# Kernel tuning notes

Measured on AMD Instinct MI355X. Metric: run time of the kernel, lower is better.

Reference implementation:

```python
import jax, jax.numpy as jnp
import numpy as np

B, IN_DIM, C, H, W = 4, 64, 128, 64, 64
HW = H * W
EPS = 1e-5


def _conv(x, w, b, pad):
    y = jax.lax.conv_general_dilated(
        x, w, (1, 1), [(pad, pad), (pad, pad)],
        dimension_numbers=('NCHW', 'OIHW', 'NCHW'))
    return y + b[None, :, None, None]


def _ln_chw(x, g, b):
    # torch LayerNorm([C,H,W]): normalize over (C,H,W) per sample, affine per-element
    m = jnp.mean(x, axis=(1, 2, 3), keepdims=True)
    v = jnp.mean((x - m) ** 2, axis=(1, 2, 3), keepdims=True)
    return (x - m) * jax.lax.rsqrt(v + EPS) * g[None] + b[None]


def _lrelu(x):
    return jnp.where(x >= 0, x, 0.01 * x)


def setup_inputs():
    ks = jax.random.split(jax.random.key(0), 16)

    def n(i, shape, s):
        return jax.random.normal(ks[i], shape, jnp.float32) * s

    inp = {
        'f_e': n(0, (B, IN_DIM, H, W), 1.0),
        'f_i': n(1, (B, IN_DIM, H, W), 1.0),
        'w1': n(2, (C, IN_DIM, 3, 3), 0.04), 'b1': jnp.zeros((C,), jnp.float32),
        'g1': jnp.ones((C, H, W), jnp.float32), 'be1': jnp.zeros((C, H, W), jnp.float32),
        'w2': n(3, (C, IN_DIM, 3, 3), 0.04), 'b2': jnp.zeros((C,), jnp.float32),
        'g2': jnp.ones((C, H, W), jnp.float32), 'be2': jnp.zeros((C, H, W), jnp.float32),
        'W3': n(4, (HW, HW), 0.015), 'b3': jnp.zeros((HW,), jnp.float32),
        'W4': n(5, (C, C), 0.08), 'b4': jnp.zeros((C,), jnp.float32),
        'W5': n(6, (C, C), 0.08), 'b5': jnp.zeros((C,), jnp.float32),
        'w6a': n(7, (C, C, 1, 1), 0.08), 'b6a': jnp.zeros((C,), jnp.float32),
        'g6a': jnp.ones((C, H, W), jnp.float32), 'be6a': jnp.zeros((C, H, W), jnp.float32),
        'w6b': n(8, (C, C, 3, 3), 0.03), 'b6b': jnp.zeros((C,), jnp.float32),
        'g6b': jnp.ones((C, H, W), jnp.float32), 'be6b': jnp.zeros((C, H, W), jnp.float32),
        'wf': n(9, (IN_DIM, C, 1, 1), 0.08), 'bf': jnp.zeros((IN_DIM,), jnp.float32),
    }
    return inp


def reference(f_e, f_i, w1, b1, g1, be1, w2, b2, g2, be2, W3, b3, W4, b4,
              W5, b5, w6a, b6a, g6a, be6a, w6b, b6b, g6b, be6b, wf, bf):
    b_, _, h, w = f_e.shape
    c = w1.shape[0]
    hw = h * w

    # f_1: conv3x3 -> LN([C,H,W]) -> LeakyReLU -> b (hw) c
    x1 = _lrelu(_ln_chw(_conv(f_e, w1, b1, 1), g1, be1))
    f_e_1 = x1.transpose(0, 2, 3, 1).reshape(b_, hw, c)

    # f_2: conv3x3 -> LN -> LeakyReLU (stays b c h w)
    f_i_2 = _lrelu(_ln_chw(_conv(f_i, w2, b2, 1), g2, be2))

    # f_3: b c (hw) -> Linear(HW,HW) -> LeakyReLU
    f_i_3 = _lrelu(jnp.einsum('bcn,mn->bcm', f_i_2.reshape(b_, c, hw), W3) + b3)

    # f_4: b (hw) c -> Linear(C,C) -> LeakyReLU
    tok = f_i_2.transpose(0, 2, 3, 1).reshape(b_, hw, c)
    f_e_4 = _lrelu(jnp.einsum('bnc,dc->bnd', tok, W4) + b4)

    # unscaled single-head attention over hw tokens
    scores = jnp.einsum('bnc,bcm->bnm', f_e_4, f_i_3)   # (b, hw, hw)
    attn = jax.nn.softmax(scores, axis=-1)
    f_e_5_in = jnp.einsum('bnm,bmc->bnc', attn, f_e_1)

    # f_5: Linear(C,C) -> LeakyReLU -> b c h w
    f_e_5 = _lrelu(jnp.einsum('bnc,dc->bnd', f_e_5_in, W5) + b5)
    f_e_5 = f_e_5.reshape(b_, h, w, c).transpose(0, 3, 1, 2)

    # f_6: conv1x1 -> LN -> LReLU -> conv3x3 -> LN -> LReLU
    y = _lrelu(_ln_chw(_conv(f_i_2, w6a, b6a, 0), g6a, be6a))
    f_i_6 = _lrelu(_ln_chw(_conv(y, w6b, b6b, 1), g6b, be6b))

    f_e_7 = f_e_5 * f_i_6
    f_e_8 = _conv(f_e_7, wf, bf, 0)
    return (f_e_8, f_i_2)
```

## Files before the change

### kernel.cpp

```cpp
#include <hip/hip_runtime.h>

typedef unsigned short ushort_t;
typedef unsigned int uint_t;
typedef unsigned long long u64_t;

#define Bn 4
#define IND 64
#define Cn 128
#define Nn 4096
#define CN 524288
#define BUF 2097152

typedef __attribute__((ext_vector_type(8))) __bf16 bf16x8;
typedef __attribute__((ext_vector_type(4))) float f32x4;

__device__ __forceinline__ float b2f(ushort_t s) {
    return __uint_as_float(((uint_t)s) << 16);
}
__device__ __forceinline__ ushort_t f2b(float f) {
    uint_t u = __float_as_uint(f);
    uint_t r = u + 0x7fffu + ((u >> 16) & 1u);
    return (ushort_t)(r >> 16);
}
__device__ __forceinline__ void unpack8(uint4 u, float* f) {
    f[0] = __uint_as_float(u.x << 16); f[1] = __uint_as_float(u.x & 0xffff0000u);
    f[2] = __uint_as_float(u.y << 16); f[3] = __uint_as_float(u.y & 0xffff0000u);
    f[4] = __uint_as_float(u.z << 16); f[5] = __uint_as_float(u.z & 0xffff0000u);
    f[6] = __uint_as_float(u.w << 16); f[7] = __uint_as_float(u.w & 0xffff0000u);
}
__device__ __forceinline__ float lrelu(float x) { return x >= 0.f ? x : 0.01f * x; }

__device__ __forceinline__ float getv(const float* p, size_t i) { return p[i]; }
__device__ __forceinline__ float getv(const ushort_t* p, size_t i) { return b2f(p[i]); }
__device__ __forceinline__ float4 get4(const float* p, size_t i) { return *(const float4*)(p + i); }
__device__ __forceinline__ float4 get4(const ushort_t* p, size_t i) {
    ushort4 u = *(const ushort4*)(p + i);
    float4 f = {b2f(u.x), b2f(u.y), b2f(u.z), b2f(u.w)};
    return f;
}
__device__ __forceinline__ void stv(float* p, float v) { *p = v; }
__device__ __forceinline__ void stv(ushort_t* p, float v) { *p = f2b(v); }

__device__ __forceinline__ uint4 pack8(float4 a, float4 b) {
    uint4 r;
    r.x = (uint_t)f2b(a.x) | ((uint_t)f2b(a.y) << 16);
    r.y = (uint_t)f2b(a.z) | ((uint_t)f2b(a.w) << 16);
    r.z = (uint_t)f2b(b.x) | ((uint_t)f2b(b.y) << 16);
    r.w = (uint_t)f2b(b.z) | ((uint_t)f2b(b.w) << 16);
    return r;
}

__global__ void detect_kernel(const void* g1, int* flag) {
    if (threadIdx.x == 0 && blockIdx.x == 0)
        *flag = (((const ushort_t*)g1)[0] == 0x3F80) ? 0 : 1;
}

template <int CI>
__global__ __launch_bounds__(256) void wtrans(const void* w, ushort_t* Wt, const int* flagp) {
    int F = *flagp;
    int idx = blockIdx.x * 256 + threadIdx.x;
    if (idx >= 128 * 9 * CI) return;
    int co = idx / (9 * CI);
    int rem = idx - co * 9 * CI;
    int tap = rem / CI;
    int ci = rem - tap * CI;
    size_t srci = (size_t)co * CI * 9 + (size_t)ci * 9 + tap;
    float v = F ? ((const float*)w)[srci] : b2f(((const ushort_t*)w)[srci]);
    Wt[idx] = f2b(v);
}

template <typename TEXT>
__device__ __forceinline__ void tin_body(const TEXT* src, ushort_t* dst, float (*tile)[33]) {
    int b = blockIdx.z, c0 = blockIdx.y * 32, n0 = blockIdx.x * 32;
    int nx = threadIdx.x & 31, cy = threadIdx.x >> 5;
    #pragma unroll
    for (int s = 0; s < 4; s++) {
        int cl = cy + s * 8;
        tile[cl][nx] = getv(src, ((size_t)(b * 64 + c0 + cl)) * 4096 + n0 + nx);
    }
    __syncthreads();
    #pragma unroll
    for (int s = 0; s < 4; s++) {
        int nl = cy + s * 8;
        dst[((size_t)b * 4096 + n0 + nl) * 64 + c0 + nx] = f2b(tile[nx][nl]);
    }
}

__global__ __launch_bounds__(256) void transpose_in(const void* src, ushort_t* dst, const int* flagp) {
    __shared__ float tile[32][33];
    int F = *flagp;
    if (F) tin_body((const float*)src, dst, tile);
    else   tin_body((const ushort_t*)src, dst, tile);
}

template <int CI>
__global__ __launch_bounds__(512) void conv_mfma(const ushort_t* __restrict__ Xt,
                                                 const ushort_t* __restrict__ Wt,
                                                 const void* bias, float* __restrict__ out,
                                                 const int* flagp) {
    constexpr int RS = CI + 8;
    constexpr int SROWS = 195;
    constexpr int SBYTES = SROWS * RS * 2;
    constexpr int OBYTES = 128 * 68 * 4;
    constexpr int SMEM = SBYTES > OBYTES ? SBYTES : OBYTES;
    __shared__ __align__(16) char smem[SMEM];
    ushort_t* S = (ushort_t*)smem;
    float* Ob = (float*)smem;

    int t = threadIdx.x;
    int blk = blockIdx.x;
    int b = blk >> 6, y = blk & 63;
    int n0 = y << 6;

    constexpr int RQ = CI / 8;
    constexpr int CNT = SROWS * RQ;
    for (int i = t; i < CNT; i += 512) {
        int s = i / RQ;
        int c8 = (i - s * RQ) * 8;
        int tok = n0 + s - 65;
        uint4 v = {0u, 0u, 0u, 0u};
        if (s < 194 && (unsigned)tok < 4096u)
            v = *(const uint4*)(Xt + ((size_t)b * 4096 + tok) * CI + c8);
        *(uint4*)(S + (size_t)s * RS + c8) = v;
    }
    __syncthreads();

    int lane = t & 63, w = t >> 6;
    int li = lane & 15, q = lane >> 4;
    int px0 = 16 * (w & 3);
    int coh = 64 * (w >> 2);
    int x = px0 + li;

    f32x4 acc[4];
    #pragma unroll
    for (int T = 0; T < 4; T++) acc[T] = {0.f, 0.f, 0.f, 0.f};

    #pragma unroll
    for (int tap = 0; tap < 9; tap++) {
        int dy = tap / 3 - 1, dx = tap % 3 - 1;
        bool vx = (unsigned)(x + dx) < 64u;
        int srow = x + dy * 64 + dx + 65;
        int sr2 = vx ? srow : 194;
        #pragma unroll
        for (int ks = 0; ks < CI / 32; ks++) {
            bf16x8 a = *(const bf16x8*)(S + (size_t)sr2 * RS + ks * 32 + q * 8);
            #pragma unroll
            for (int T = 0; T < 4; T++) {
                int co = coh + 16 * T + li;
                bf16x8 bb = *(const bf16x8*)(Wt + ((size_t)co * 9 + tap) * CI + ks * 32 + q * 8);
                acc[T] = __builtin_amdgcn_mfma_f32_16x16x32_bf16(a, bb, acc[T], 0, 0, 0);
            }
        }
    }
    __syncthreads();

    int F = *flagp;
    #pragma unroll
    for (int T = 0; T < 4; T++) {
        int co = coh + 16 * T + li;
        float bv = F ? ((const float*)bias)[co] : b2f(((const ushort_t*)bias)[co]);
        #pragma unroll
        for (int rr = 0; rr < 4; rr++)
            Ob[(size_t)co * 68 + px0 + 4 * q + rr] = acc[T][rr] + bv;
    }
    __syncthreads();
    for (int i = t; i < 2048; i += 512) {
        int co = i >> 4, p4 = (i & 15) * 4;
        *(uint4*)(out + ((size_t)(b * 128 + co)) * 4096 + n0 + p4) =
            *(const uint4*)(Ob + (size_t)co * 68 + p4);
    }
}

__global__ __launch_bounds__(256) void ln_reduce1(const float* __restrict__ src,
                                                  float* __restrict__ part) {
    int t = threadIdx.x;
    size_t base = (size_t)blockIdx.x * 1024 + t * 4;
    float4 v = *(const float4*)(src + base);
    float s = v.x + v.y + v.z + v.w;
    float q = v.x * v.x + v.y * v.y + v.z * v.z + v.w * v.w;
    for (int off = 32; off > 0; off >>= 1) {
        s += __shfl_down(s, off, 64);
        q += __shfl_down(q, off, 64);
    }
    __shared__ float red[8];
    if ((t & 63) == 0) { red[(t >> 6) * 2] = s; red[(t >> 6) * 2 + 1] = q; }
    __syncthreads();
    if (t == 0) {
        s = red[0] + red[2] + red[4] + red[6];
        q = red[1] + red[3] + red[5] + red[7];
        part[blockIdx.x * 2] = s;
        part[blockIdx.x * 2 + 1] = q;
    }
}

__global__ __launch_bounds__(256) void ln_reduce2(const float* __restrict__ part,
                                                  float* __restrict__ der) {
    int b = blockIdx.x, t = threadIdx.x;
    float s = part[(b * 512 + t) * 2] + part[(b * 512 + 256 + t) * 2];
    float q = part[(b * 512 + t) * 2 + 1] + part[(b * 512 + 256 + t) * 2 + 1];
    for (int off = 32; off > 0; off >>= 1) {
        s += __shfl_down(s, off, 64);
        q += __shfl_down(q, off, 64);
    }
    __shared__ float red[8];
    if ((t & 63) == 0) { red[(t >> 6) * 2] = s; red[(t >> 6) * 2 + 1] = q; }
    __syncthreads();
    if (t == 0) {
        s = red[0] + red[2] + red[4] + red[6];
        q = red[1] + red[3] + red[5] + red[7];
        float mean = s * (1.f / (float)CN);
        float var = q * (1.f / (float)CN) - mean * mean;
        der[b * 2] = mean;
        der[b * 2 + 1] = rsqrtf(var + 1e-5f);
    }
}

template <typename TEXT, typename TOD, int HT, int HD>
__device__ __forceinline__ void ln_body(const float* src, const TEXT* g, const TEXT* be,
                                        const float* der, ushort_t* outT, TOD* outD,
                                        float (*tile)[33]) {
    int b = blockIdx.z, c0 = blockIdx.y * 32, n0 = blockIdx.x * 32;
    float mean = der[b * 2], rstd = der[b * 2 + 1];
    int nx = threadIdx.x & 31, cy = threadIdx.x >> 5;
    #pragma unroll
    for (int s = 0; s < 4; s++) {
        int cl = cy + s * 8;
        int c = c0 + cl;
        size_t gi = (size_t)c * Nn + n0 + nx;
        float v = (src[(size_t)b * CN + gi] - mean) * rstd * getv(g, gi) + getv(be, gi);
        v = lrelu(v);
        if (HD) stv(outD + (size_t)b * CN + gi, v);
        tile[cl][nx] = v;
    }
    if (HT) {
        __syncthreads();
        #pragma unroll
        for (int s = 0; s < 4; s++) {
            int nl = cy + s * 8;
            int n = n0 + nl;
            int c = c0 + nx;
            outT[((size_t)b * Nn + n) * Cn + c] = f2b(tile[nx][nl]);
        }
    }
}

template <int HT, int HD, int DEXT>
__global__ __launch_bounds__(256) void ln_apply(const float* src, const void* g, const void* be,
                                                const float* der, ushort_t* outT, void* outD,
                                                long doff, const int* flagp) {
    __shared__ float tile[32][33];
    int F = *flagp;
    if (F) {
        if (DEXT && HD)
            ln_body<float, float, HT, HD>(src, (const float*)g, (const float*)be, der, outT,
                                          ((float*)outD) + doff, tile);
        else
            ln_body<float, ushort_t, HT, HD>(src, (const float*)g, (const float*)be, der, outT,
                                             ((ushort_t*)outD) + doff, tile);
    } else {
        ln_body<ushort_t, ushort_t, HT, HD>(src, (const ushort_t*)g, (const ushort_t*)be, der, outT,
                                            ((ushort_t*)outD) + doff, tile);
    }
}

template <int ACT, int TRANS, typename TA, typename TW, typename TO>
__device__ __forceinline__ void gemm_body(const TA* A, const TW* W, const TW* bias, TO* out,
                                          int M, int K, int Rper,
                                          float (*As)[68], float (*Bs)[68]) {
    int m0 = blockIdx.x << 6, r0 = blockIdx.y << 6;
    int t = threadIdx.x, tx = t & 15, ty = t >> 4;
    int sr = t >> 2, sk = (t & 3) << 2;
    float acc[4][4] = {{0.f}};
    for (int kt = 0; kt < K; kt += 16) {
        float4 av = get4(A, (size_t)(r0 + sr) * K + kt + sk);
        float4 wv = get4(W, (size_t)(m0 + sr) * K + kt + sk);
        As[sk + 0][sr] = av.x; As[sk + 1][sr] = av.y;
        As[sk + 2][sr] = av.z; As[sk + 3][sr] = av.w;
        Bs[sk + 0][sr] = wv.x; Bs[sk + 1][sr] = wv.y;
        Bs[sk + 2][sr] = wv.z; Bs[sk + 3][sr] = wv.w;
        __syncthreads();
        #pragma unroll
        for (int kk = 0; kk < 16; kk++) {
            float4 a4 = *(const float4*)&As[kk][ty << 2];
            float4 b4 = *(const float4*)&Bs[kk][tx << 2];
            float aa[4] = {a4.x, a4.y, a4.z, a4.w};
            float bb[4] = {b4.x, b4.y, b4.z, b4.w};
            #pragma unroll
            for (int ii = 0; ii < 4; ii++)
                #pragma unroll
                for (int jj = 0; jj < 4; jj++)
                    acc[ii][jj] += aa[ii] * bb[jj];
        }
        __syncthreads();
    }
    float bv[4];
    #pragma unroll
    for (int jj = 0; jj < 4; jj++) bv[jj] = getv(bias, m0 + (tx << 2) + jj);
    #pragma unroll
    for (int ii = 0; ii < 4; ii++) {
        int r = r0 + (ty << 2) + ii;
        float v[4];
        #pragma unroll
        for (int jj = 0; jj < 4; jj++) {
            float x = acc[ii][jj] + bv[jj];
            if (ACT) x = lrelu(x);
            v[jj] = x;
        }
        if (TRANS) {
            int rb = r / Rper, ri = r % Rper;
            #pragma unroll
            for (int jj = 0; jj < 4; jj++) {
                int m = m0 + (tx << 2) + jj;
                stv(out + ((size_t)rb * M + m) * Rper + ri, v[jj]);
            }
        } else {
            #pragma unroll
            for (int jj = 0; jj < 4; jj++)
                stv(out + (size_t)r * M + m0 + (tx << 2) + jj, v[jj]);
        }
    }
}

template <int ACT, int TRANS, int AK, typename TO>
__global__ __launch_bounds__(256) void gemm_nt(const void* A, long aoff, const void* W,
                                               const void* bias, TO* out, int M, int K, int Rper,
                                               const int* flagp) {
    __shared__ float As[16][68];
    __shared__ float Bs[16][68];
    int F = *flagp;
    if (AK == 0) {
        if (F) gemm_body<ACT, TRANS>((const ushort_t*)A + aoff, (const float*)W, (const float*)bias, out, M, K, Rper, As, Bs);
        else   gemm_body<ACT, TRANS>((const ushort_t*)A + aoff, (const ushort_t*)W, (const ushort_t*)bias, out, M, K, Rper, As, Bs);
    } else if (AK == 1) {
        if (F) gemm_body<ACT, TRANS>((const float*)A + aoff, (const float*)W, (const float*)bias, out, M, K, Rper, As, Bs);
        else   gemm_body<ACT, TRANS>((const float*)A + aoff, (const ushort_t*)W, (const ushort_t*)bias, out, M, K, Rper, As, Bs);
    } else {
        if (F) gemm_body<ACT, TRANS>((const float*)A + aoff, (const float*)W, (const float*)bias, out, M, K, Rper, As, Bs);
        else   gemm_body<ACT, TRANS>((const ushort_t*)A + aoff, (const ushort_t*)W, (const ushort_t*)bias, out, M, K, Rper, As, Bs);
    }
}

template <typename TA, typename TW>
__device__ __forceinline__ void gemm_big_body(const TA* A, const TW* W3, const TW* b3,
                                              ushort_t* out, char* smem) {
    ushort_t* As = (ushort_t*)smem;
    ushort_t* Bs = (ushort_t*)(smem + 9216);
    int t = threadIdx.x;
    int m0 = blockIdx.x << 7;
    int r0 = blockIdx.y << 6;
    int lane = t & 63, w = t >> 6;
    int li = lane & 15, q = lane >> 4;
    int rs = 16 * (w & 3);
    int mh = 64 * (w >> 2);
    f32x4 acc[4];
    #pragma unroll
    for (int T = 0; T < 4; T++) acc[T] = {0.f, 0.f, 0.f, 0.f};

    int ar = t >> 3, ak8 = (t & 7) * 8;
    int br = t >> 2, bk16 = (t & 3) * 16;

    {
        size_t abase = (size_t)(r0 + ar) * 4096 + ak8;
        *(uint4*)(As + (size_t)ar * 72 + ak8) = pack8(get4(A, abase), get4(A, abase + 4));
        size_t bbase = (size_t)(m0 + br) * 4096 + bk16;
        *(uint4*)(Bs + (size_t)br * 72 + bk16) = pack8(get4(W3, bbase), get4(W3, bbase + 4));
        *(uint4*)(Bs + (size_t)br * 72 + bk16 + 8) = pack8(get4(W3, bbase + 8), get4(W3, bbase + 12));
    }
    __syncthreads();

    for (int kt = 0; kt < 4096; kt += 64) {
        float4 pa0, pa1, pb0, pb1, pb2, pb3;
        bool pf = kt < 4032;
        if (pf) {
            size_t abase = (size_t)(r0 + ar) * 4096 + kt + 64 + ak8;
            pa0 = get4(A, abase); pa1 = get4(A, abase + 4);
            size_t bbase = (size_t)(m0 + br) * 4096 + kt + 64 + bk16;
            pb0 = get4(W3, bbase); pb1 = get4(W3, bbase + 4);
            pb2 = get4(W3, bbase + 8); pb3 = get4(W3, bbase + 12);
        }
        #pragma unroll
        for (int ks = 0; ks < 2; ks++) {
            bf16x8 a = *(const bf16x8*)(As + (size_t)(rs + li) * 72 + ks * 32 + q * 8);
            #pragma unroll
            for (int T = 0; T < 4; T++) {
                bf16x8 bb = *(const bf16x8*)(Bs + (size_t)(mh + 16 * T + li) * 72 + ks * 32 + q * 8);
                acc[T] = __builtin_amdgcn_mfma_f32_16x16x32_bf16(a, bb, acc[T], 0, 0, 0);
            }
        }
        __syncthreads();
        if (pf) {
            *(uint4*)(As + (size_t)ar * 72 + ak8) = pack8(pa0, pa1);
            *(uint4*)(Bs + (size_t)br * 72 + bk16) = pack8(pb0, pb1);
            *(uint4*)(Bs + (size_t)br * 72 + bk16 + 8) = pack8(pb2, pb3);
        }
        __syncthreads();
    }

    ushort_t* Ob = (ushort_t*)smem;
    #pragma unroll
    for (int T = 0; T < 4; T++) {
        int m_l = mh + 16 * T + li;
        float bv = getv(b3, m0 + m_l);
        #pragma unroll
        for (int rr = 0; rr < 4; rr++) {
            float v = lrelu(acc[T][rr] + bv);
            Ob[(size_t)m_l * 72 + rs + 4 * q + rr] = f2b(v);
        }
    }
    __syncthreads();
    int b = r0 >> 7;
    int c0 = ((r0 >> 6) & 1) * 64;
    for (int i = t; i < 1024; i += 512) {
        int m_l = i >> 3, c8 = (i & 7) * 8;
        *(uint4*)(out + ((size_t)b * 4096 + m0 + m_l) * 128 + c0 + c8) =
            *(const uint4*)(Ob + (size_t)m_l * 72 + c8);
    }
}

__global__ __launch_bounds__(512) void gemm_big(const void* A, long aoff, const void* W3,
                                                const void* b3, ushort_t* out, const int* flagp) {
    __shared__ __align__(16) char smem[27648];
    int F = *flagp;
    if (F) gemm_big_body((const float*)A + aoff, (const float*)W3, (const float*)b3, out, smem);
    else   gemm_big_body((const ushort_t*)A + aoff, (const ushort_t*)W3, (const ushort_t*)b3, out, smem);
}

__global__ __launch_bounds__(256) void attn_mfma(const ushort_t* __restrict__ Q,
                                                 const ushort_t* __restrict__ Kg,
                                                 const ushort_t* __restrict__ Vg,
                                                 float* __restrict__ Og) {
    __shared__ __align__(16) ushort_t Qs[64 * 136];
    __shared__ __align__(16) ushort_t Ks[64 * 136];
    __shared__ __align__(16) ushort_t Ps[64 * 72];
    __shared__ __align__(16) ushort_t Vt[128 * 68];

    int t = threadIdx.x;
    int blk = blockIdx.x;
    int b = (blk >> 1) & 3;
    int qt = ((blk >> 3) << 1) | (blk & 1);
    int n0 = qt << 6;
    int lane = t & 63, w = t >> 6;
    int li = lane & 15, q = lane >> 4;

    int kj = t >> 2, kc0 = (t & 3) * 32;
    int vd = t >> 1, vk0 = (t & 1) * 32;

    {
        const ushort_t* qp = Q + ((size_t)(b * Nn + n0 + kj)) * 128 + kc0;
        ushort_t* dst = Qs + kj * 136 + kc0;
        #pragma unroll
        for (int cc = 0; cc < 4; cc++)
            *(uint4*)(dst + cc * 8) = *(const uint4*)(qp + cc * 8);
    }
    {
        const ushort_t* kp = Kg + ((size_t)(b * Nn + kj)) * 128 + kc0;
        ushort_t* dst = Ks + kj * 136 + kc0;
        #pragma unroll
        for (int cc = 0; cc < 4; cc++)
            *(uint4*)(dst + cc * 8) = *(const uint4*)(kp + cc * 8);
    }
    {
        const ushort_t* vp = Vg + (size_t)b * CN + (size_t)vd * Nn + vk0;
        ushort_t* dst = Vt + vd * 68 + vk0;
        #pragma unroll
        for (int cc = 0; cc < 4; cc++) {
            uint4 v = *(const uint4*)(vp + cc * 8);
            uint2 lo = {v.x, v.y}, hi = {v.z, v.w};
            *(uint2*)(dst + cc * 8) = lo;
            *(uint2*)(dst + cc * 8 + 4) = hi;
        }
    }

    f32x4 acc[8];
    #pragma unroll
    for (int T = 0; T < 8; T++) acc[T] = {0.f, 0.f, 0.f, 0.f};
    float m_i[4], l_i[4];
    #pragma unroll
    for (int r = 0; r < 4; r++) { m_i[r] = -1e30f; l_i[r] = 0.f; }

    __syncthreads();

    for (int kt = 0; kt < 64; kt++) {
        uint4 pk[4], pv[4];
        bool pf = kt < 63;
        if (pf) {
            int m1 = (kt + 1) << 6;
            const ushort_t* kp = Kg + ((size_t)(b * Nn + m1 + kj)) * 128 + kc0;
            #pragma unroll
            for (int cc = 0; cc < 4; cc++) pk[cc] = *(const uint4*)(kp + cc * 8);
            const ushort_t* vp = Vg + (size_t)b * CN + (size_t)vd * Nn + m1 + vk0;
            #pragma unroll
            for (int cc = 0; cc < 4; cc++) pv[cc] = *(const uint4*)(vp + cc * 8);
        }

        f32x4 s[4];
        #pragma unroll
        for (int T = 0; T < 4; T++) s[T] = {0.f, 0.f, 0.f, 0.f};
        #pragma unroll
        for (int ks = 0; ks < 4; ks++) {
            bf16x8 a = *(const bf16x8*)(Qs + (16 * w + li) * 136 + ks * 32 + q * 8);
            #pragma unroll
            for (int T = 0; T < 4; T++) {
                bf16x8 bb = *(const bf16x8*)(Ks + (16 * T + li) * 136 + ks * 32 + q * 8);
                s[T] = __builtin_amdgcn_mfma_f32_16x16x32_bf16(a, bb, s[T], 0, 0, 0);
            }
        }

        float alpha[4];
        float p[4][4];
        #pragma unroll
        for (int r = 0; r < 4; r++) {
            float rm = fmaxf(fmaxf(s[0][r], s[1][r]), fmaxf(s[2][r], s[3][r]));
            rm = fmaxf(rm, __shfl_xor(rm, 1, 64));
            rm = fmaxf(rm, __shfl_xor(rm, 2, 64));
            rm = fmaxf(rm, __shfl_xor(rm, 4, 64));
            rm = fmaxf(rm, __shfl_xor(rm, 8, 64));
            float mnew = fmaxf(m_i[r], rm);
            alpha[r] = __expf(m_i[r] - mnew);
            m_i[r] = mnew;
            float rsum = 0.f;
            #pragma unroll
            for (int T = 0; T < 4; T++) {
                float pvv = __expf(s[T][r] - mnew);
                p[T][r] = pvv;
                rsum += pvv;
            }
            rsum += __shfl_xor(rsum, 1, 64);
            rsum += __shfl_xor(rsum, 2, 64);
            rsum += __shfl_xor(rsum, 4, 64);
            rsum += __shfl_xor(rsum, 8, 64);
            l_i[r] = l_i[r] * alpha[r] + rsum;
        }
        #pragma unroll
        for (int T = 0; T < 4; T++)
            #pragma unroll
            for (int r = 0; r < 4; r++)
                Ps[(16 * w + 4 * q + r) * 72 + 16 * T + li] = f2b(p[T][r]);

        #pragma unroll
        for (int T = 0; T < 8; T++)
            #pragma unroll
            for (int r = 0; r < 4; r++)
                acc[T][r] *= alpha[r];
        #pragma unroll
        for (int ks = 0; ks < 2; ks++) {
            bf16x8 a = *(const bf16x8*)(Ps + (16 * w + li) * 72 + ks * 32 + q * 8);
            #pragma unroll
            for (int T = 0; T < 8; T++) {
                const ushort_t* vb = Vt + (16 * T + li) * 68 + ks * 32 + q * 8;
                union { u64_t u[2]; bf16x8 v; } bv;
                bv.u[0] = *(const u64_t*)(vb);
                bv.u[1] = *(const u64_t*)(vb + 4);
                acc[T] = __builtin_amdgcn_mfma_f32_16x16x32_bf16(a, bv.v, acc[T], 0, 0, 0);
            }
        }
        __syncthreads();
        if (pf) {
            ushort_t* dk = Ks + kj * 136 + kc0;
            #pragma unroll
            for (int cc = 0; cc < 4; cc++) *(uint4*)(dk + cc * 8) = pk[cc];
            ushort_t* dv = Vt + vd * 68 + vk0;
            #pragma unroll
            for (int cc = 0; cc < 4; cc++) {
                uint2 lo = {pv[cc].x, pv[cc].y}, hi = {pv[cc].z, pv[cc].w};
                *(uint2*)(dv + cc * 8) = lo;
                *(uint2*)(dv + cc * 8 + 4) = hi;
            }
            __syncthreads();
        }
    }

    float inv[4];
    #pragma unroll
    for (int r = 0; r < 4; r++) inv[r] = 1.f / l_i[r];
    #pragma unroll
    for (int T = 0; T < 8; T++)
        #pragma unroll
        for (int r = 0; r < 4; r++) {
            int n = n0 + 16 * w + 4 * q + r;
            int d = 16 * T + li;
            Og[((size_t)(b * Nn + n)) * 128 + d] = acc[T][r] * inv[r];
        }
}

template <typename TEXT, typename TOUT>
__device__ __forceinline__ void final_body(const ushort_t* fe5, const ushort_t* fi6t,
                                           const TEXT* wf, const TEXT* bf, TOUT* out0,
                                           float* prod, ushort_t* wfs, float* bfs) {
    int t = threadIdx.x;
    int b = blockIdx.x >> 6;
    int px0 = (blockIdx.x & 63) * 64;
    for (int idx = t * 4; idx < 8192; idx += 1024) {
        float4 v = get4(wf, idx);
        ushort4 u = {f2b(v.x), f2b(v.y), f2b(v.z), f2b(v.w)};
        *(ushort4*)&wfs[idx] = u;
    }
    if (t < 64) bfs[t] = getv(bf, t);
    {
        int pix = t >> 2, kc = (t & 3) * 32;
        const ushort_t* ap = fe5 + ((size_t)(b * Nn + px0 + pix)) * 128 + kc;
        const ushort_t* bp = fi6t + ((size_t)(b * Nn + px0 + pix)) * 128 + kc;
        #pragma unroll
        for (int c = 0; c < 4; c++) {
            uint4 ua = *(const uint4*)(ap + c * 8);
            uint4 ub = *(const uint4*)(bp + c * 8);
            float fa[8], fb[8];
            unpack8(ua, fa);
            unpack8(ub, fb);
            float* pp = &prod[pix * 132 + kc + c * 8];
            #pragma unroll
            for (int j = 0; j < 8; j++) pp[j] = fa[j] * fb[j];
        }
    }
    __syncthreads();
    int pix = t >> 2, og = t & 3;
    for (int k = 0; k < 16; k++) {
        int o = og * 16 + k;
        float a = bfs[o];
        for (int kc = 0; kc < 128; kc += 8) {
            uint4 wu = *(const uint4*)&wfs[o * 128 + kc];
            float w8[8];
            unpack8(wu, w8);
            const float* pp = &prod[pix * 132 + kc];
            float4 p0 = *(const float4*)pp;
            float4 p1 = *(const float4*)(pp + 4);
            a += w8[0] * p0.x + w8[1] * p0.y + w8[2] * p0.z + w8[3] * p0.w
               + w8[4] * p1.x + w8[5] * p1.y + w8[6] * p1.z + w8[7] * p1.w;
        }
        stv(out0 + ((size_t)(b * 64 + o)) * Nn + px0 + pix, a);
    }
}

__global__ __launch_bounds__(256) void final_out(const ushort_t* fe5, const ushort_t* fi6t,
                                                 const void* wf, const void* bf, void* out0,
                                                 const int* flagp) {
    __shared__ __align__(16) float prod[64 * 132];
    __shared__ __align__(16) ushort_t wfs[64 * 128];
    __shared__ float bfs[64];
    int F = *flagp;
    if (F) final_body((const ushort_t*)fe5, fi6t, (const float*)wf, (const float*)bf, (float*)out0, prod, wfs, bfs);
    else   final_body((const ushort_t*)fe5, fi6t, (const ushort_t*)wf, (const ushort_t*)bf, (ushort_t*)out0, prod, wfs, bfs);
}

extern "C" void kernel_launch(void* const* d_in, const int* in_sizes, int n_in,
                              void* d_out, int out_size, void* d_ws, size_t ws_size,
                              hipStream_t stream) {
    const void* f_e = d_in[0];
    const void* f_i = d_in[1];
    const void* w1 = d_in[2];
    const void* b1 = d_in[3];
    const void* g1 = d_in[4];
    const void* be1 = d_in[5];
    const void* w2 = d_in[6];
    const void* b2 = d_in[7];
    const void* g2 = d_in[8];
    const void* be2 = d_in[9];
    const void* W3 = d_in[10];
    const void* b3 = d_in[11];
    const void* W4 = d_in[12];
    const void* b4 = d_in[13];
    const void* W5 = d_in[14];
    const void* b5 = d_in[15];
    const void* w6a = d_in[16];
    const void* b6a = d_in[17];
    const void* g6a = d_in[18];
    const void* be6a = d_in[19];
    const void* w6b = d_in[20];
    const void* b6b = d_in[21];
    const void* g6b = d_in[22];
    const void* be6b = d_in[23];
    const void* wf = d_in[24];
    const void* bf = d_in[25];

    char* wsb = (char*)d_ws;
    int* FLAG = (int*)wsb;
    float* PART = (float*)(wsb + 1024);
    float* DER  = (float*)(wsb + 17408);
    ushort_t* Wt1  = (ushort_t*)(wsb + 32768);
    ushort_t* Wt2  = (ushort_t*)(wsb + 180224);
    ushort_t* Wt6b = (ushort_t*)(wsb + 327680);
    float* TMP  = (float*)(wsb + 622592);
    ushort_t* FE1  = (ushort_t*)(wsb + 9011200);
    ushort_t* TOK  = FE1 + BUF;
    ushort_t* FI3T = TOK + BUF;
    ushort_t* FE4  = FI3T + BUF;
    ushort_t* Y6   = FE4 + BUF;
    ushort_t* FI6T = Y6 + BUF;

    ushort_t* FEt = FI3T;
    ushort_t* FIt = FE4;

    const long OUT1OFF = (long)Bn * IND * Nn;

    dim3 lnGrid(128, 4, 4);
    dim3 tinGrid(128, 2, 4);

    detect_kernel<<<1, 64, 0, stream>>>(g1, FLAG);

    wtrans<64><<<288, 256, 0, stream>>>(w1, Wt1, FLAG);
    wtrans<64><<<288, 256, 0, stream>>>(w2, Wt2, FLAG);
    wtrans<128><<<576, 256, 0, stream>>>(w6b, Wt6b, FLAG);

    transpose_in<<<tinGrid, 256, 0, stream>>>(f_e, FEt, FLAG);
    conv_mfma<64><<<256, 512, 0, stream>>>(FEt, Wt1, b1, TMP, FLAG);
    ln_reduce1<<<2048, 256, 0, stream>>>(TMP, PART);
    ln_reduce2<<<4, 256, 0, stream>>>(PART, DER);
    ln_apply<0, 1, 0><<<lnGrid, 256, 0, stream>>>(TMP, g1, be1, DER, nullptr, FE1, 0, FLAG);

    transpose_in<<<tinGrid, 256, 0, stream>>>(f_i, FIt, FLAG);
    conv_mfma<64><<<256, 512, 0, stream>>>(FIt, Wt2, b2, TMP, FLAG);
    ln_reduce1<<<2048, 256, 0, stream>>>(TMP, PART);
    ln_reduce2<<<4, 256, 0, stream>>>(PART, DER);
    ln_apply<1, 1, 1><<<lnGrid, 256, 0, stream>>>(TMP, g2, be2, DER, TOK, d_out, OUT1OFF, FLAG);

    gemm_big<<<dim3(32, 8), 512, 0, stream>>>(d_out, OUT1OFF, W3, b3, FI3T, FLAG);

    gemm_nt<1, 0, 0, ushort_t><<<dim3(2, 256), 256, 0, stream>>>(TOK, 0, W4, b4, FE4, 128, 128, 1, FLAG);

    gemm_nt<0, 1, 0, float><<<dim3(2, 256), 256, 0, stream>>>(TOK, 0, w6a, b6a, TMP, 128, 128, 4096, FLAG);
    ln_reduce1<<<2048, 256, 0, stream>>>(TMP, PART);
    ln_reduce2<<<4, 256, 0, stream>>>(PART, DER);
    ln_apply<1, 0, 0><<<lnGrid, 256, 0, stream>>>(TMP, g6a, be6a, DER, Y6, nullptr, 0, FLAG);

    conv_mfma<128><<<256, 512, 0, stream>>>(Y6, Wt6b, b6b, TMP, FLAG);
    ln_reduce1<<<2048, 256, 0, stream>>>(TMP, PART);
    ln_reduce2<<<4, 256, 0, stream>>>(PART, DER);
    ln_apply<1, 0, 0><<<lnGrid, 256, 0, stream>>>(TMP, g6b, be6b, DER, FI6T, nullptr, 0, FLAG);

    attn_mfma<<<256, 256, 0, stream>>>(FE4, FI3T, FE1, TMP);

    gemm_nt<1, 0, 1, ushort_t><<<dim3(2, 256), 256, 0, stream>>>(TMP, 0, W5, b5, Y6, 128, 128, 1, FLAG);

    final_out<<<256, 256, 0, stream>>>(Y6, FI6T, wf, bf, d_out, FLAG);
}
```

Before: 607.3 us.

## Split attention KV range in two and merge partial results

Splits the attention key/value loop into two halves handled by separate blocks, doubling the grid from 256 to 512 blocks. Each half writes unnormalized bf16 partial outputs plus per-row max and sum, and a new merge kernel combines them with log-sum-exp rescaling into the fp32 output. This targets low occupancy on a GPU with many compute units, at the cost of an extra kernel launch, extra memory traffic, and bf16 rounding of the unnormalized partial accumulators. The P tile's shared-memory stride also changes from 72 to 80.

New measurement: 592.7 us. 2.4% less time.

```diff
diff --git a/kernel.cpp b/kernel.cpp
--- a/kernel.cpp
+++ b/kernel.cpp
@@ -428,16 +428,20 @@
 __global__ __launch_bounds__(256) void attn_mfma(const ushort_t* __restrict__ Q,
                                                  const ushort_t* __restrict__ Kg,
                                                  const ushort_t* __restrict__ Vg,
-                                                 float* __restrict__ Og) {
+                                                 ushort_t* __restrict__ Op0,
+                                                 ushort_t* __restrict__ Op1,
+                                                 float* __restrict__ ML) {
     __shared__ __align__(16) ushort_t Qs[64 * 136];
     __shared__ __align__(16) ushort_t Ks[64 * 136];
-    __shared__ __align__(16) ushort_t Ps[64 * 72];
+    __shared__ __align__(16) ushort_t Ps[64 * 80];
     __shared__ __align__(16) ushort_t Vt[128 * 68];
 
     int t = threadIdx.x;
     int blk = blockIdx.x;
-    int b = (blk >> 1) & 3;
-    int qt = ((blk >> 3) << 1) | (blk & 1);
+    int h = blk >> 8;
+    int rblk = blk & 255;
+    int b = (rblk >> 1) & 3;
+    int qt = ((rblk >> 3) << 1) | (rblk & 1);
     int n0 = qt << 6;
     int lane = t & 63, w = t >> 6;
     int li = lane & 15, q = lane >> 4;
@@ -445,6 +449,9 @@
     int kj = t >> 2, kc0 = (t & 3) * 32;
     int vd = t >> 1, vk0 = (t & 1) * 32;
 
+    int kt0 = h << 5;
+    int m00 = kt0 << 6;
+
     {
         const ushort_t* qp = Q + ((size_t)(b * Nn + n0 + kj)) * 128 + kc0;
         ushort_t* dst = Qs + kj * 136 + kc0;
@@ -453,14 +460,14 @@
             *(uint4*)(dst + cc * 8) = *(const uint4*)(qp + cc * 8);
     }
     {
-        const ushort_t* kp = Kg + ((size_t)(b * Nn + kj)) * 128 + kc0;
+        const ushort_t* kp = Kg + ((size_t)(b * Nn + m00 + kj)) * 128 + kc0;
         ushort_t* dst = Ks + kj * 136 + kc0;
         #pragma unroll
         for (int cc = 0; cc < 4; cc++)
             *(uint4*)(dst + cc * 8) = *(const uint4*)(kp + cc * 8);
     }
     {
-        const ushort_t* vp = Vg + (size_t)b * CN + (size_t)vd * Nn + vk0;
+        const ushort_t* vp = Vg + (size_t)b * CN + (size_t)vd * Nn + m00 + vk0;
         ushort_t* dst = Vt + vd * 68 + vk0;
         #pragma unroll
         for (int cc = 0; cc < 4; cc++) {
@@ -480,9 +487,9 @@
 
     __syncthreads();
 
-    for (int kt = 0; kt < 64; kt++) {
+    for (int kt = kt0; kt < kt0 + 32; kt++) {
         uint4 pk[4], pv[4];
-        bool pf = kt < 63;
+        bool pf = kt < kt0 + 31;
         if (pf) {
             int m1 = (kt + 1) << 6;
             const ushort_t* kp = Kg + ((size_t)(b * Nn + m1 + kj)) * 128 + kc0;
@@ -535,7 +542,7 @@
         for (int T = 0; T < 4; T++)
             #pragma unroll
             for (int r = 0; r < 4; r++)
-                Ps[(16 * w + 4 * q + r) * 72 + 16 * T + li] = f2b(p[T][r]);
+                Ps[(16 * w + 4 * q + r) * 80 + 16 * T + li] = f2b(p[T][r]);
 
         #pragma unroll
         for (int T = 0; T < 8; T++)
@@ -544,7 +551,7 @@
                 acc[T][r] *= alpha[r];
         #pragma unroll
         for (int ks = 0; ks < 2; ks++) {
-            bf16x8 a = *(const bf16x8*)(Ps + (16 * w + li) * 72 + ks * 32 + q * 8);
+            bf16x8 a = *(const bf16x8*)(Ps + (16 * w + li) * 80 + ks * 32 + q * 8);
             #pragma unroll
             for (int T = 0; T < 8; T++) {
                 const ushort_t* vb = Vt + (16 * T + li) * 68 + ks * 32 + q * 8;
@@ -570,17 +577,54 @@
         }
     }
 
-    float inv[4];
-    #pragma unroll
-    for (int r = 0; r < 4; r++) inv[r] = 1.f / l_i[r];
+    ushort_t* Op = h ? Op1 : Op0;
     #pragma unroll
     for (int T = 0; T < 8; T++)
         #pragma unroll
         for (int r = 0; r < 4; r++) {
             int n = n0 + 16 * w + 4 * q + r;
             int d = 16 * T + li;
-            Og[((size_t)(b * Nn + n)) * 128 + d] = acc[T][r] * inv[r];
-        }
+            Op[((size_t)(b * Nn + n)) * 128 + d] = f2b(acc[T][r]);
+        }
+    if (li == 0) {
+        #pragma unroll
+        for (int r = 0; r < 4; r++) {
+            int n = n0 + 16 * w + 4 * q + r;
+            size_t mi = ((size_t)(h * Bn + b) * Nn + n) * 2;
+            ML[mi] = m_i[r];
+            ML[mi + 1] = l_i[r];
+        }
+    }
+}
+
+__global__ __launch_bounds__(256) void attn_merge(const ushort_t* __restrict__ Op0,
+                                                  const ushort_t* __restrict__ Op1,
+                                                  const float* __restrict__ ML,
+                                                  float* __restrict__ Og) {
+    int idx = blockIdx.x * 256 + threadIdx.x;
+    int token = idx >> 4;
+    int c8 = (idx & 15) * 8;
+    float m0 = ML[(size_t)token * 2], l0 = ML[(size_t)token * 2 + 1];
+    float m1 = ML[((size_t)(4 * Nn * 4) + (size_t)token) * 2 - (size_t)(4 * Nn * 4) * 2 + (size_t)(Bn * Nn + token) * 2 - (size_t)token * 2];
+    m1 = ML[((size_t)Bn * Nn + token) * 2];
+    float l1 = ML[((size_t)Bn * Nn + token) * 2 + 1];
+    float M = fmaxf(m0, m1);
+    float e0 = __expf(m0 - M), e1 = __expf(m1 - M);
+    float denom = l0 * e0 + l1 * e1;
+    float s0 = e0 / denom, s1 = e1 / denom;
+    uint4 u0 = *(const uint4*)(Op0 + (size_t)token * 128 + c8);
+    uint4 u1 = *(const uint4*)(Op1 + (size_t)token * 128 + c8);
+    float f0[8], f1[8];
+    unpack8(u0, f0);
+    unpack8(u1, f1);
+    float o[8];
+    #pragma unroll
+    for (int j = 0; j < 8; j++) o[j] = f0[j] * s0 + f1[j] * s1;
+    float4 v0 = {o[0], o[1], o[2], o[3]};
+    float4 v1 = {o[4], o[5], o[6], o[7]};
+    float* op = Og + (size_t)token * 128 + c8;
+    *(float4*)op = v0;
+    *(float4*)(op + 4) = v1;
 }
 
 template <typename TEXT, typename TOUT>
@@ -679,6 +723,7 @@
     ushort_t* Wt1  = (ushort_t*)(wsb + 32768);
     ushort_t* Wt2  = (ushort_t*)(wsb + 180224);
     ushort_t* Wt6b = (ushort_t*)(wsb + 327680);
+    float* ML   = (float*)(wsb + 32768);
     float* TMP  = (float*)(wsb + 622592);
     ushort_t* FE1  = (ushort_t*)(wsb + 9011200);
     ushort_t* TOK  = FE1 + BUF;
@@ -727,7 +772,8 @@
     ln_reduce2<<<4, 256, 0, stream>>>(PART, DER);
     ln_apply<1, 0, 0><<<lnGrid, 256, 0, stream>>>(TMP, g6b, be6b, DER, FI6T, nullptr, 0, FLAG);
 
-    attn_mfma<<<256, 256, 0, stream>>>(FE4, FI3T, FE1, TMP);
+    attn_mfma<<<512, 256, 0, stream>>>(FE4, FI3T, FE1, TOK, Y6, ML);
+    attn_merge<<<1024, 256, 0, stream>>>(TOK, Y6, ML, TMP);
 
     gemm_nt<1, 0, 1, ushort_t><<<dim3(2, 256), 256, 0, stream>>>(TMP, 0, W5, b5, Y6, 128, 128, 1, FLAG);
 
```
